# Performance work log

Measured on AMD Instinct MI355X. Metric: run time of the kernel, lower is better.

Reference implementation:

```python
import jax, jax.numpy as jnp
import numpy as np

N_NODES = 50000
N_EDGES = 800000
DIM = 64


def _param(key, shape, scale):
    return jax.random.normal(key, shape, dtype=jnp.float32) * scale


def setup_inputs() -> dict:
    key = jax.random.key(0)
    ks = jax.random.split(key, 20)
    s = 1.0 / np.sqrt(DIM)
    x = jax.random.normal(ks[0], (N_NODES, DIM), dtype=jnp.float32)
    weights = jax.random.uniform(ks[1], (6,), dtype=jnp.float32)
    edge_index = jax.random.randint(ks[2], (2, N_EDGES), 0, N_NODES, dtype=jnp.int64)
    return {
        "x": x,
        "weights": weights,
        # mlp
        "W_mlp": _param(ks[3], (DIM, DIM), s), "b_mlp": jnp.zeros((DIM,), jnp.float32),
        # sage (mean aggregator): lin_l on neighbor mean, lin_r on self
        "Wl_sage": _param(ks[4], (DIM, DIM), s), "Wr_sage": _param(ks[5], (DIM, DIM), s),
        "b_sage": jnp.zeros((DIM,), jnp.float32),
        # gcn
        "W_gcn": _param(ks[6], (DIM, DIM), s), "b_gcn": jnp.zeros((DIM,), jnp.float32),
        # gat (single head)
        "W_gat": _param(ks[7], (DIM, DIM), s),
        "a_src": _param(ks[8], (DIM,), s), "a_dst": _param(ks[9], (DIM,), s),
        "b_gat": jnp.zeros((DIM,), jnp.float32),
        # chebconv K=3
        "W_cheb": _param(ks[10], (3, DIM, DIM), s), "b_cheb": jnp.zeros((DIM,), jnp.float32),
        # gin (eps=0, nn = Linear)
        "W_gin": _param(ks[11], (DIM, DIM), s), "b_gin": jnp.zeros((DIM,), jnp.float32),
        "edge_index": edge_index,
    }


def _mixed_forward(x, weights, W_mlp, b_mlp, Wl_sage, Wr_sage, b_sage,
                   W_gcn, b_gcn, W_gat, a_src, a_dst, b_gat,
                   W_cheb, b_cheb, W_gin, b_gin, edge_index):
    N = x.shape[0]
    src, dst = edge_index[0], edge_index[1]
    seg_sum = lambda v, idx: jax.ops.segment_sum(v, idx, num_segments=N)

    deg = seg_sum(jnp.ones(src.shape[0], x.dtype), dst)  # in-degree [N]
    nsum = seg_sum(x[src], dst)                           # sum of neighbor feats [N, D]

    # --- mlp (graph-free) ---
    o_mlp = x @ W_mlp + b_mlp

    # --- sage, mean aggregation ---
    nmean = nsum / jnp.maximum(deg, 1.0)[:, None]
    o_sage = nmean @ Wl_sage + x @ Wr_sage + b_sage

    # --- gcn with self loops: D'^{-1/2} (A+I) D'^{-1/2} X W ---
    dinv = jax.lax.rsqrt(deg + 1.0)
    xw = x @ W_gcn
    norm_e = dinv[src] * dinv[dst]
    o_gcn = seg_sum(norm_e[:, None] * xw[src], dst) + xw * (dinv * dinv)[:, None] + b_gcn

    # --- gat, single head, self loops appended, leaky_relu(0.2) scoring ---
    h = x @ W_gat
    el, er = h @ a_src, h @ a_dst
    loop = jnp.arange(N, dtype=src.dtype)
    src2 = jnp.concatenate([src, loop])
    dst2 = jnp.concatenate([dst, loop])
    e = jax.nn.leaky_relu(el[src2] + er[dst2], 0.2)
    m = jax.ops.segment_max(e, dst2, num_segments=N)
    p = jnp.exp(e - m[dst2])
    z = jax.ops.segment_sum(p, dst2, num_segments=N)
    alpha = p / (z[dst2] + 1e-16)
    o_gat = jax.ops.segment_sum(alpha[:, None] * h[src2], dst2, num_segments=N) + b_gat

    # --- cheb K=3, lambda_max=2: L_hat = L_norm - I = -A_norm ---
    dinv_c = jax.lax.rsqrt(jnp.maximum(deg, 1.0))
    nrm = dinv_c[src] * dinv_c[dst]
    prop = lambda t: seg_sum(nrm[:, None] * t[src], dst)
    T0 = x
    T1 = -prop(T0)
    T2 = -2.0 * prop(T1) - T0
    o_cheb = T0 @ W_cheb[0] + T1 @ W_cheb[1] + T2 @ W_cheb[2] + b_cheb

    # --- gin, eps=0, nn = Linear ---
    o_gin = (x + nsum) @ W_gin + b_gin

    outs = (o_mlp, o_sage, o_gcn, o_gat, o_cheb, o_gin)
    res = jnp.zeros_like(o_mlp)
    for k, o in enumerate(outs):
        res = res + weights[k] * jax.nn.elu(o)
    return res


def reference(x, weights, W_mlp, b_mlp, Wl_sage, Wr_sage, b_sage,
              W_gcn, b_gcn, W_gat, a_src, a_dst, b_gat,
              W_cheb, b_cheb, W_gin, b_gin, edge_index):
    return _mixed_forward(x, weights, W_mlp, b_mlp, Wl_sage, Wr_sage, b_sage,
                          W_gcn, b_gcn, W_gat, a_src, a_dst, b_gat,
                          W_cheb, b_cheb, W_gin, b_gin, edge_index)
```

## Files before the change

### kernel.cpp

```cpp
#include <hip/hip_runtime.h>
#include <cstdint>
#include <cstddef>

#define NN 50000
#define NE 800000
#define CAP 96
#define NSEG 8
#define SEGW 6250

constexpr size_t O_CNT   = 0;
constexpr size_t O_SLOT  = 50048;
constexpr size_t O_NODAL = O_SLOT + (size_t)NN*CAP;
constexpr size_t O_VA    = O_NODAL + 200000;
constexpr size_t O_VB    = O_VA + 64;
constexpr size_t O_XB    = O_VB + 64;
constexpr size_t O_NSB   = O_XB + 1600032;
constexpr size_t O_T1B   = O_NSB + 1600000;
constexpr size_t O_V1B   = O_T1B + 1600032;
constexpr size_t O_GB    = O_V1B + 1600000;
constexpr size_t O_WPK   = O_GB  + 1600000;

typedef __attribute__((ext_vector_type(8))) short short8;
typedef __attribute__((ext_vector_type(4))) float f32x4;

__device__ __forceinline__ float leaky02(float v){ return v >= 0.f ? v : 0.2f*v; }
__device__ __forceinline__ float eluf(float v){ return v > 0.f ? v : (__expf(v) - 1.f); }

__device__ __forceinline__ void lds_fence(){
  asm volatile("s_waitcnt lgkmcnt(0)" ::: "memory");
}

__device__ __forceinline__ unsigned short f2bf(float f){
  unsigned u = __float_as_uint(f);
  unsigned r = (u + 0x7FFFu + ((u >> 16) & 1u)) >> 16;
  return (unsigned short)r;
}
__device__ __forceinline__ float bf2f(unsigned short b){
  return __uint_as_float(((unsigned)b) << 16);
}
__device__ __forceinline__ unsigned pack2(unsigned short lo, unsigned short hi){
  return (unsigned)lo | ((unsigned)hi << 16);
}

__global__ __launch_bounds__(256) void k_scatter(
    const int* __restrict__ src, const int* __restrict__ dst,
    int* __restrict__ cnt, unsigned short* __restrict__ slot,
    const float* __restrict__ W_mlp, const float* __restrict__ Wr,
    const float* __restrict__ W_cheb, const float* __restrict__ W_gin,
    const float* __restrict__ Wl, const float* __restrict__ W_gcn,
    const float* __restrict__ W_gat,
    const float* __restrict__ a_src, const float* __restrict__ a_dst,
    const float4* __restrict__ x4,
    float* __restrict__ va, float* __restrict__ vb,
    unsigned short* __restrict__ wpk,
    ushort4* __restrict__ xb4, ushort4* __restrict__ t1b4){
  int b = blockIdx.x;
  int seg = b & (NSEG-1);
  int lo = seg * SEGW;
  int e = (b >> 3)*256 + threadIdx.x;
  if (e < NE){
    int d = dst[e];
    if ((unsigned)(d - lo) < (unsigned)SEGW){
      int s = src[e];
      int pos = atomicAdd(&cnt[d], 1);
      if (pos < CAP) slot[(size_t)d*CAP + pos] = (unsigned short)s;
    }
  }
  if (b == 0){
    int k = threadIdx.x;
    if (k < 64){
      float sa = 0.f, sb = 0.f;
      for (int j = 0; j < 64; ++j){
        float w = W_gat[k*64 + j];
        sa = fmaf(w, a_src[j], sa);
        sb = fmaf(w, a_dst[j], sb);
      }
      va[k] = sa; vb[k] = sb;
    }
  } else if (b <= 9){
    int w = b - 1;
    const float* s; const float* sub = nullptr;
    switch (w){
      case 0: s = W_mlp; break;
      case 1: s = Wr; break;
      case 2: s = W_cheb; sub = W_cheb + 8192; break;
      case 3: s = W_gin; break;
      case 4: s = Wl; break;
      case 5: s = W_cheb + 4096; break;
      case 6: s = W_cheb + 8192; break;
      case 7: s = W_gcn; break;
      default: s = W_gat; break;
    }
    for (int ee = threadIdx.x; ee < 4096; ee += 256){
      int k = ee >> 6, n = ee & 63;
      float f = s[ee];
      if (sub) f -= sub[ee];
      wpk[(size_t)w*4096 + (size_t)n*64 + k] = f2bf(f);
    }
  } else if (b < 3136){
    int i = (b - 10)*256 + threadIdx.x;
    if (i < NN*16){
      float4 v = x4[i];
      ushort4 o;
      o.x = f2bf(v.x); o.y = f2bf(v.y); o.z = f2bf(v.z); o.w = f2bf(v.w);
      xb4[i] = o;
    } else if (i < (NN+1)*16){
      ushort4 z; z.x = 0; z.y = 0; z.z = 0; z.w = 0;
      xb4[i] = z;
      t1b4[i] = z;
    }
  }
}

__global__ __launch_bounds__(256) void k_nodal(const unsigned short* __restrict__ xb,
    const int* __restrict__ cnt, const float* __restrict__ va, const float* __restrict__ vb,
    float4* __restrict__ nodal){
  int tid = threadIdx.x;
  int li = tid & 15;
  int row = blockIdx.x*16 + (tid >> 4);
  if (row >= NN) return;
  ushort4 hb = *(const ushort4*)&xb[(size_t)row*64 + li*4];
  float4 hv = make_float4(bf2f(hb.x), bf2f(hb.y), bf2f(hb.z), bf2f(hb.w));
  float4 av = *(const float4*)&va[li*4];
  float4 bv = *(const float4*)&vb[li*4];
  float ps = hv.x*av.x + hv.y*av.y + hv.z*av.z + hv.w*av.w;
  float pd = hv.x*bv.x + hv.y*bv.y + hv.z*bv.z + hv.w*bv.w;
  #pragma unroll
  for (int o = 1; o < 16; o <<= 1){ ps += __shfl_xor(ps, o); pd += __shfl_xor(pd, o); }
  if (li == 0){
    float c = (float)cnt[row];
    float dinv  = rsqrtf(c + 1.f);
    float dinvc = rsqrtf(fmaxf(c, 1.f));
    nodal[row] = make_float4(dinvc, dinv, ps, pd);
  }
}

__global__ __launch_bounds__(256) void k_aggA(
    const unsigned short* __restrict__ xb,
    const int* __restrict__ cnt, const unsigned short* __restrict__ slot,
    const float4* __restrict__ nodal,
    unsigned* __restrict__ nsb2, unsigned* __restrict__ t1b2,
    unsigned* __restrict__ v1b2, unsigned* __restrict__ gb2){
  __shared__ float4 sW[4][64];
  int wid  = threadIdx.x >> 6;
  int lane = threadIdx.x & 63;
  int half = lane >> 5, hl = lane & 31;
  int node = blockIdx.x*8 + wid*2 + half;
  int c = min(cnt[node], CAP);
  int cmax = max(c, __shfl_xor(c, 32));
  const unsigned short* sl = slot + (size_t)node*CAP;
  float4 nn = nodal[node];
  float ern = nn.w;
  float a0e=0.f,a0o=0.f,a1e=0.f,a1o=0.f,a2e=0.f,a2o=0.f,a3e=0.f,a3o=0.f, zl=0.f;
  for (int base = 0; base < cmax; base += 32){
    int rem = c - base;
    bool act = hl < rem;
    int s = act ? (int)sl[base+hl] : NN;
    float4 ns = act ? nodal[s] : make_float4(0.f,0.f,0.f,0.f);
    float p = act ? __expf(fminf(leaky02(ns.z + ern), 60.f)) : 0.f;
    zl += p;
    sW[wid][lane] = make_float4(__int_as_float(s), ns.x, ns.y, p);
    lds_fence();
    int remw = min(32, cmax - base);
    for (int j = 0; j < remw; j += 8){
      float4 w[8]; unsigned uv[8];
      #pragma unroll
      for (int q2 = 0; q2 < 8; ++q2){
        w[q2] = sW[wid][half*32 + j + q2];
        int sb = __float_as_int(w[q2].x);
        sb = ((unsigned)sb <= (unsigned)NN) ? sb : NN;
        uv[q2] = *(const unsigned*)&xb[(size_t)sb*64 + 2*hl];
      }
      #pragma unroll
      for (int q2 = 0; q2 < 8; ++q2){
        float lo = __uint_as_float(uv[q2] << 16);
        float hi = __uint_as_float(uv[q2] & 0xffff0000u);
        a0e += lo;                       a0o += hi;
        a1e = fmaf(w[q2].y, lo, a1e);    a1o = fmaf(w[q2].y, hi, a1o);
        a2e = fmaf(w[q2].z, lo, a2e);    a2o = fmaf(w[q2].z, hi, a2o);
        a3e = fmaf(w[q2].w, lo, a3e);    a3o = fmaf(w[q2].w, hi, a3o);
      }
    }
    lds_fence();
  }
  #pragma unroll
  for (int o = 1; o <= 16; o <<= 1) zl += __shfl_xor(zl, o);
  unsigned uxs = *(const unsigned*)&xb[(size_t)node*64 + 2*hl];
  float xsx = __uint_as_float(uxs << 16);
  float xsy = __uint_as_float(uxs & 0xffff0000u);
  float p_self = __expf(fminf(leaky02(nn.z + nn.w), 60.f));
  float rz = 1.f / (zl + p_self + 1e-16f);
  size_t off2 = (size_t)node*32 + hl;
  nsb2[off2] = pack2(f2bf(a0e), f2bf(a0o));
  t1b2[off2] = pack2(f2bf(-nn.x*a1e), f2bf(-nn.x*a1o));
  v1b2[off2] = pack2(f2bf(nn.y*a2e + nn.y*nn.y*xsx), f2bf(nn.y*a2o + nn.y*nn.y*xsy));
  gb2[off2]  = pack2(f2bf((a3e + p_self*xsx)*rz), f2bf((a3o + p_self*xsy)*rz));
}

__global__ __launch_bounds__(256) void k_aggBepi(
    const unsigned short* __restrict__ t1b,
    const int* __restrict__ cnt, const unsigned short* __restrict__ slot,
    const float4* __restrict__ nodal,
    const float* __restrict__ wts,
    const float* __restrict__ b_mlp, const float* __restrict__ b_sage,
    const float* __restrict__ b_gcn, const float* __restrict__ b_gat,
    const float* __restrict__ b_cheb, const float* __restrict__ b_gin,
    const unsigned short* __restrict__ wpk,
    const unsigned short* __restrict__ xb, const unsigned short* __restrict__ nsb,
    const unsigned short* __restrict__ v1b, const unsigned short* __restrict__ gb,
    float* __restrict__ out){
  __shared__ float2 sW0[4][64], sW1[4][64];
  __shared__ unsigned ubl[16][32];
  const int tid  = threadIdx.x;
  const int wid  = tid >> 6;
  const int lane = tid & 63;
  const int half = lane >> 5, hl = lane & 31;
  const int rowbase = blockIdx.x * 16;

  {
    const int r0 = wid*4 + half*2;
    const int n0 = rowbase + r0;
    const int n1 = n0 + 1;
    int c0 = min(cnt[n0], CAP), c1 = min(cnt[n1], CAP);
    int cm = max(c0, c1);
    cm = max(cm, __shfl_xor(cm, 32));
    const unsigned short* sl0 = slot + (size_t)n0*CAP;
    const unsigned short* sl1 = slot + (size_t)n1*CAP;
    const float* nf = (const float*)nodal;
    float ae0=0.f, ao0=0.f, ae1=0.f, ao1=0.f;
    for (int base = 0; base < cm; base += 32){
      bool a0 = hl < (c0 - base), a1 = hl < (c1 - base);
      int s0 = a0 ? (int)sl0[base+hl] : NN;
      int s1 = a1 ? (int)sl1[base+hl] : NN;
      float d0 = a0 ? nf[(size_t)s0*4] : 0.f;
      float d1 = a1 ? nf[(size_t)s1*4] : 0.f;
      sW0[wid][lane] = make_float2(__int_as_float(s0), d0);
      sW1[wid][lane] = make_float2(__int_as_float(s1), d1);
      lds_fence();
      int remw = min(32, cm - base);
      for (int j = 0; j < remw; j += 8){
        float2 w0[8], w1[8]; unsigned uv0[8], uv1[8];
        #pragma unroll
        for (int k = 0; k < 8; ++k){
          w0[k] = sW0[wid][half*32 + j + k];
          w1[k] = sW1[wid][half*32 + j + k];
          int sb0 = __float_as_int(w0[k].x);
          sb0 = ((unsigned)sb0 <= (unsigned)NN) ? sb0 : NN;
          int sb1 = __float_as_int(w1[k].x);
          sb1 = ((unsigned)sb1 <= (unsigned)NN) ? sb1 : NN;
          uv0[k] = *(const unsigned*)&t1b[(size_t)sb0*64 + 2*hl];
          uv1[k] = *(const unsigned*)&t1b[(size_t)sb1*64 + 2*hl];
        }
        #pragma unroll
        for (int k = 0; k < 8; ++k){
          float lo0 = __uint_as_float(uv0[k] << 16), hi0 = __uint_as_float(uv0[k] & 0xffff0000u);
          float lo1 = __uint_as_float(uv1[k] << 16), hi1 = __uint_as_float(uv1[k] & 0xffff0000u);
          ae0 = fmaf(w0[k].y, lo0, ae0); ao0 = fmaf(w0[k].y, hi0, ao0);
          ae1 = fmaf(w1[k].y, lo1, ae1); ao1 = fmaf(w1[k].y, hi1, ao1);
        }
      }
      lds_fence();
    }
    float sc0 = -2.f * nodal[n0].x;
    float sc1 = -2.f * nodal[n1].x;
    ubl[r0  ][hl ^ (((r0  )&7)<<2)] = pack2(f2bf(sc0*ae0), f2bf(sc0*ao0));
    ubl[r0+1][hl ^ (((r0+1)&7)<<2)] = pack2(f2bf(sc1*ae1), f2bf(sc1*ao1));
  }
  __syncthreads();

  const int ml = lane & 15;
  const int q  = lane >> 4;
  const float w0 = wts[0], w1 = wts[1], w2 = wts[2], w3 = wts[3], w4 = wts[4], w5 = wts[5];
  const float* nod = (const float*)nodal;

  short8 ah0, ah1;
  auto loadA = [&](const unsigned short* __restrict__ src){
    const unsigned short* p = src + (size_t)(rowbase + ml)*64 + q*8;
    ah0 = *(const short8*)p;
    ah1 = *(const short8*)(p + 32);
  };
  auto groupOne = [&](int w, f32x4& acc){
    const unsigned short* bp = wpk + (size_t)w*4096 + (size_t)(wid*16 + ml)*64;
    short8 b0 = *(const short8*)(bp + q*8);
    short8 b1 = *(const short8*)(bp + 32 + q*8);
    acc = __builtin_amdgcn_mfma_f32_16x16x32_bf16(ah0, b0, acc, 0, 0, 0);
    acc = __builtin_amdgcn_mfma_f32_16x16x32_bf16(ah1, b1, acc, 0, 0, 0);
  };

  f32x4 res = (f32x4){0.f,0.f,0.f,0.f};
  auto emit1 = [&](const f32x4& acc, const float* __restrict__ bias, float wk){
    float b = bias[wid*16 + ml];
    #pragma unroll
    for (int r = 0; r < 4; ++r) res[r] += wk * eluf(acc[r] + b);
  };

  {
    const unsigned* rp = ubl[ml];
    int wi0 = (q*4)      ^ ((ml&7)<<2);
    int wi1 = (16 + q*4) ^ ((ml&7)<<2);
    ah0 = *(const short8*)(rp + wi0);
    ah1 = *(const short8*)(rp + wi1);
  }
  f32x4 accC = (f32x4){0.f,0.f,0.f,0.f};
  groupOne(6, accC);

  f32x4 t, accWr, accG;
  loadA(v1b); t = (f32x4){0.f,0.f,0.f,0.f};
  groupOne(7, t); emit1(t, b_gcn, w2);
  loadA(gb);  t = (f32x4){0.f,0.f,0.f,0.f};
  groupOne(8, t); emit1(t, b_gat, w3);
  loadA(t1b); groupOne(5, accC);
  loadA(xb);  t = (f32x4){0.f,0.f,0.f,0.f};
  groupOne(0, t); emit1(t, b_mlp, w0);
  accWr = (f32x4){0.f,0.f,0.f,0.f};
  groupOne(1, accWr);
  groupOne(2, accC); emit1(accC, b_cheb, w4);
  accG = (f32x4){0.f,0.f,0.f,0.f};
  groupOne(3, accG);
  loadA(nsb); groupOne(3, accG); emit1(accG, b_gin, w5);
  t = (f32x4){0.f,0.f,0.f,0.f};
  groupOne(4, t);
  {
    float b = b_sage[wid*16 + ml];
    #pragma unroll
    for (int r = 0; r < 4; ++r){
      int row = rowbase + q*4 + r;
      float dc = nod[(size_t)row*4];
      float invd = dc*dc;
      res[r] += w1 * eluf(invd*t[r] + accWr[r] + b);
    }
  }
  #pragma unroll
  for (int r = 0; r < 4; ++r){
    int row = rowbase + q*4 + r;
    out[(size_t)row*64 + wid*16 + ml] = res[r];
  }
}

extern "C" void kernel_launch(void* const* d_in, const int* in_sizes, int n_in,
                              void* d_out, int out_size, void* d_ws, size_t ws_size,
                              hipStream_t stream){
  const float* x      = (const float*)d_in[0];
  const float* wts    = (const float*)d_in[1];
  const float* W_mlp  = (const float*)d_in[2];
  const float* b_mlp  = (const float*)d_in[3];
  const float* Wl     = (const float*)d_in[4];
  const float* Wr     = (const float*)d_in[5];
  const float* b_sage = (const float*)d_in[6];
  const float* W_gcn  = (const float*)d_in[7];
  const float* b_gcn  = (const float*)d_in[8];
  const float* W_gat  = (const float*)d_in[9];
  const float* a_src  = (const float*)d_in[10];
  const float* a_dst  = (const float*)d_in[11];
  const float* b_gat  = (const float*)d_in[12];
  const float* W_cheb = (const float*)d_in[13];
  const float* b_cheb = (const float*)d_in[14];
  const float* W_gin  = (const float*)d_in[15];
  const float* b_gin  = (const float*)d_in[16];
  const int*   ei     = (const int*)d_in[17];

  float* wsf  = (float*)d_ws;
  int*  cnt   = (int*)d_ws;
  unsigned short* slot = (unsigned short*)(wsf + O_SLOT);
  float4* nodal = (float4*)(wsf + O_NODAL);
  float* va   = wsf + O_VA;
  float* vb   = wsf + O_VB;
  unsigned short* xbu = (unsigned short*)(wsf + O_XB);
  unsigned short* nsb = (unsigned short*)(wsf + O_NSB);
  unsigned short* t1b = (unsigned short*)(wsf + O_T1B);
  unsigned short* v1b = (unsigned short*)(wsf + O_V1B);
  unsigned short* gb  = (unsigned short*)(wsf + O_GB);
  unsigned short* wpk = (unsigned short*)(wsf + O_WPK);
  float* out  = (float*)d_out;

  hipMemsetAsync(cnt, 0, NN*sizeof(int), stream);
  k_scatter <<<25000,256, 0, stream>>>(ei, ei + NE, cnt, slot,
                                       W_mlp, Wr, W_cheb, W_gin, Wl, W_gcn, W_gat,
                                       a_src, a_dst, (const float4*)x,
                                       va, vb, wpk, (ushort4*)xbu, (ushort4*)t1b);
  k_nodal   <<<3125, 256, 0, stream>>>(xbu, cnt, va, vb, nodal);
  k_aggA    <<<6250, 256, 0, stream>>>(xbu, cnt, slot, nodal,
                                       (unsigned*)nsb, (unsigned*)t1b,
                                       (unsigned*)v1b, (unsigned*)gb);
  k_aggBepi <<<3125, 256, 0, stream>>>(t1b, cnt, slot, nodal,
                                       wts, b_mlp, b_sage, b_gcn, b_gat, b_cheb, b_gin,
                                       wpk, xbu, nsb, v1b, gb, out);
}
```

Measured before the change: 221.8 us.

## Interleave node blocks across XCD segments and prefetch MFMA operands early

Blocks in both aggregation kernels are remapped so that consecutive block IDs (which the hardware spreads round-robin over the 8 XCDs) work on contiguous node segments of 6250 nodes each. Each XCD's L2 then sees a localized node range, and padding guards handle partial tiles. In the epilogue kernel, all five bf16 A-operand tiles are loaded into registers before the gather phase, so their latency overlaps the neighbor aggregation instead of stalling later. This costs more registers and adds bounds checks, and the gathered neighbours are random, so locality may improve only for the per-node writes and reads.

Result: no change. 223.5 us (+0.8%).

```diff
diff --git a/kernel.cpp b/kernel.cpp
--- a/kernel.cpp
+++ b/kernel.cpp
@@ -145,8 +145,13 @@
   int wid  = threadIdx.x >> 6;
   int lane = threadIdx.x & 63;
   int half = lane >> 5, hl = lane & 31;
-  int node = blockIdx.x*8 + wid*2 + half;
-  int c = min(cnt[node], CAP);
+  int b    = blockIdx.x;
+  int seg  = b & (NSEG-1);
+  int idx  = b >> 3;
+  int lbase = idx*8 + wid*2 + half;
+  bool vld = lbase < SEGW;
+  int node = seg*SEGW + (vld ? lbase : 0);
+  int c = vld ? min(cnt[node], CAP) : 0;
   int cmax = max(c, __shfl_xor(c, 32));
   const unsigned short* sl = slot + (size_t)node*CAP;
   float4 nn = nodal[node];
@@ -190,11 +195,13 @@
   float xsy = __uint_as_float(uxs & 0xffff0000u);
   float p_self = __expf(fminf(leaky02(nn.z + nn.w), 60.f));
   float rz = 1.f / (zl + p_self + 1e-16f);
-  size_t off2 = (size_t)node*32 + hl;
-  nsb2[off2] = pack2(f2bf(a0e), f2bf(a0o));
-  t1b2[off2] = pack2(f2bf(-nn.x*a1e), f2bf(-nn.x*a1o));
-  v1b2[off2] = pack2(f2bf(nn.y*a2e + nn.y*nn.y*xsx), f2bf(nn.y*a2o + nn.y*nn.y*xsy));
-  gb2[off2]  = pack2(f2bf((a3e + p_self*xsx)*rz), f2bf((a3o + p_self*xsy)*rz));
+  if (vld){
+    size_t off2 = (size_t)node*32 + hl;
+    nsb2[off2] = pack2(f2bf(a0e), f2bf(a0o));
+    t1b2[off2] = pack2(f2bf(-nn.x*a1e), f2bf(-nn.x*a1o));
+    v1b2[off2] = pack2(f2bf(nn.y*a2e + nn.y*nn.y*xsx), f2bf(nn.y*a2o + nn.y*nn.y*xsy));
+    gb2[off2]  = pack2(f2bf((a3e + p_self*xsx)*rz), f2bf((a3o + p_self*xsy)*rz));
+  }
 }
 
 __global__ __launch_bounds__(256) void k_aggBepi(
@@ -215,13 +222,31 @@
   const int wid  = tid >> 6;
   const int lane = tid & 63;
   const int half = lane >> 5, hl = lane & 31;
-  const int rowbase = blockIdx.x * 16;
+  const int b    = blockIdx.x;
+  const int seg  = b & (NSEG-1);
+  const int idx  = b >> 3;
+  const int rowbase = seg*SEGW + idx*16;
+  const int nvalid  = min(16, SEGW - idx*16);
+
+  const int ml = lane & 15;
+  const int q  = lane >> 4;
+  short8 Av1[2], Agb[2], At1[2], Ax[2], Ans[2];
+  {
+    const size_t ro = (size_t)(rowbase + ml)*64 + q*8;
+    Av1[0] = *(const short8*)(v1b + ro); Av1[1] = *(const short8*)(v1b + ro + 32);
+    Agb[0] = *(const short8*)(gb  + ro); Agb[1] = *(const short8*)(gb  + ro + 32);
+    At1[0] = *(const short8*)(t1b + ro); At1[1] = *(const short8*)(t1b + ro + 32);
+    Ax[0]  = *(const short8*)(xb  + ro); Ax[1]  = *(const short8*)(xb  + ro + 32);
+    Ans[0] = *(const short8*)(nsb + ro); Ans[1] = *(const short8*)(nsb + ro + 32);
+  }
 
   {
     const int r0 = wid*4 + half*2;
-    const int n0 = rowbase + r0;
-    const int n1 = n0 + 1;
-    int c0 = min(cnt[n0], CAP), c1 = min(cnt[n1], CAP);
+    const bool v0 = r0 < nvalid, v1r = (r0+1) < nvalid;
+    const int n0 = rowbase + (v0 ? r0 : 0);
+    const int n1 = rowbase + (v1r ? r0+1 : 0);
+    int c0 = v0  ? min(cnt[n0], CAP) : 0;
+    int c1 = v1r ? min(cnt[n1], CAP) : 0;
     int cm = max(c0, c1);
     cm = max(cm, __shfl_xor(cm, 32));
     const unsigned short* sl0 = slot + (size_t)n0*CAP;
@@ -268,72 +293,67 @@
   }
   __syncthreads();
 
-  const int ml = lane & 15;
-  const int q  = lane >> 4;
   const float w0 = wts[0], w1 = wts[1], w2 = wts[2], w3 = wts[3], w4 = wts[4], w5 = wts[5];
   const float* nod = (const float*)nodal;
 
-  short8 ah0, ah1;
-  auto loadA = [&](const unsigned short* __restrict__ src){
-    const unsigned short* p = src + (size_t)(rowbase + ml)*64 + q*8;
-    ah0 = *(const short8*)p;
-    ah1 = *(const short8*)(p + 32);
-  };
-  auto groupOne = [&](int w, f32x4& acc){
+  auto groupOne = [&](int w, const short8& a0, const short8& a1, f32x4& acc){
     const unsigned short* bp = wpk + (size_t)w*4096 + (size_t)(wid*16 + ml)*64;
     short8 b0 = *(const short8*)(bp + q*8);
     short8 b1 = *(const short8*)(bp + 32 + q*8);
-    acc = __builtin_amdgcn_mfma_f32_16x16x32_bf16(ah0, b0, acc, 0, 0, 0);
-    acc = __builtin_amdgcn_mfma_f32_16x16x32_bf16(ah1, b1, acc, 0, 0, 0);
+    acc = __builtin_amdgcn_mfma_f32_16x16x32_bf16(a0, b0, acc, 0, 0, 0);
+    acc = __builtin_amdgcn_mfma_f32_16x16x32_bf16(a1, b1, acc, 0, 0, 0);
   };
 
   f32x4 res = (f32x4){0.f,0.f,0.f,0.f};
   auto emit1 = [&](const f32x4& acc, const float* __restrict__ bias, float wk){
-    float b = bias[wid*16 + ml];
+    float bsv = bias[wid*16 + ml];
     #pragma unroll
-    for (int r = 0; r < 4; ++r) res[r] += wk * eluf(acc[r] + b);
+    for (int r = 0; r < 4; ++r) res[r] += wk * eluf(acc[r] + bsv);
   };
 
+  short8 Au0, Au1;
   {
     const unsigned* rp = ubl[ml];
     int wi0 = (q*4)      ^ ((ml&7)<<2);
     int wi1 = (16 + q*4) ^ ((ml&7)<<2);
-    ah0 = *(const short8*)(rp + wi0);
-    ah1 = *(const short8*)(rp + wi1);
+    Au0 = *(const short8*)(rp + wi0);
+    Au1 = *(const short8*)(rp + wi1);
   }
   f32x4 accC = (f32x4){0.f,0.f,0.f,0.f};
-  groupOne(6, accC);
+  groupOne(6, Au0, Au1, accC);
 
   f32x4 t, accWr, accG;
-  loadA(v1b); t = (f32x4){0.f,0.f,0.f,0.f};
-  groupOne(7, t); emit1(t, b_gcn, w2);
-  loadA(gb);  t = (f32x4){0.f,0.f,0.f,0.f};
-  groupOne(8, t); emit1(t, b_gat, w3);
-  loadA(t1b); groupOne(5, accC);
-  loadA(xb);  t = (f32x4){0.f,0.f,0.f,0.f};
-  groupOne(0, t); emit1(t, b_mlp, w0);
+  t = (f32x4){0.f,0.f,0.f,0.f};
+  groupOne(7, Av1[0], Av1[1], t); emit1(t, b_gcn, w2);
+  t = (f32x4){0.f,0.f,0.f,0.f};
+  groupOne(8, Agb[0], Agb[1], t); emit1(t, b_gat, w3);
+  groupOne(5, At1[0], At1[1], accC);
+  t = (f32x4){0.f,0.f,0.f,0.f};
+  groupOne(0, Ax[0], Ax[1], t); emit1(t, b_mlp, w0);
   accWr = (f32x4){0.f,0.f,0.f,0.f};
-  groupOne(1, accWr);
-  groupOne(2, accC); emit1(accC, b_cheb, w4);
+  groupOne(1, Ax[0], Ax[1], accWr);
+  groupOne(2, Ax[0], Ax[1], accC); emit1(accC, b_cheb, w4);
   accG = (f32x4){0.f,0.f,0.f,0.f};
-  groupOne(3, accG);
-  loadA(nsb); groupOne(3, accG); emit1(accG, b_gin, w5);
+  groupOne(3, Ax[0], Ax[1], accG);
+  groupOne(3, Ans[0], Ans[1], accG); emit1(accG, b_gin, w5);
   t = (f32x4){0.f,0.f,0.f,0.f};
-  groupOne(4, t);
+  groupOne(4, Ans[0], Ans[1], t);
   {
-    float b = b_sage[wid*16 + ml];
+    float bsv = b_sage[wid*16 + ml];
     #pragma unroll
     for (int r = 0; r < 4; ++r){
       int row = rowbase + q*4 + r;
       float dc = nod[(size_t)row*4];
       float invd = dc*dc;
-      res[r] += w1 * eluf(invd*t[r] + accWr[r] + b);
+      res[r] += w1 * eluf(invd*t[r] + accWr[r] + bsv);
     }
   }
   #pragma unroll
   for (int r = 0; r < 4; ++r){
-    int row = rowbase + q*4 + r;
-    out[(size_t)row*64 + wid*16 + ml] = res[r];
+    if (q*4 + r < nvalid){
+      int row = rowbase + q*4 + r;
+      out[(size_t)row*64 + wid*16 + ml] = res[r];
+    }
   }
 }
 
@@ -379,10 +399,10 @@
                                        a_src, a_dst, (const float4*)x,
                                        va, vb, wpk, (ushort4*)xbu, (ushort4*)t1b);
   k_nodal   <<<3125, 256, 0, stream>>>(xbu, cnt, va, vb, nodal);
-  k_aggA    <<<6250, 256, 0, stream>>>(xbu, cnt, slot, nodal,
+  k_aggA    <<<6256, 256, 0, stream>>>(xbu, cnt, slot, nodal,
                                        (unsigned*)nsb, (unsigned*)t1b,
                                        (unsigned*)v1b, (unsigned*)gb);
-  k_aggBepi <<<3125, 256, 0, stream>>>(t1b, cnt, slot, nodal,
+  k_aggBepi <<<3128, 256, 0, stream>>>(t1b, cnt, slot, nodal,
                                        wts, b_mlp, b_sage, b_gcn, b_gat, b_cheb, b_gin,
                                        wpk, xbu, nsb, v1b, gb, out);
 }
```
